# Optimization experiments

Hardware: AMD Instinct MI355X
Metric: run time of the kernel (lower is better)

Reference implementation:

```python
import jax, jax.numpy as jnp
import numpy as np

DELTA_V = 0.5
DELTA_D = 1.5
ALPHA = 1.0
BETA = 1.0
GAMMA = 0.001
K = 32          # max number of instance labels per image
EPS = 1e-12     # sqrt safety for masked/degenerate distances


def setup_inputs() -> dict:
    key = jax.random.key(0)
    k1, k2 = jax.random.split(key)
    B, F, H, W = 8, 32, 512, 512
    embeds = jax.random.normal(k1, (B, F, H, W), dtype=jnp.float32)
    labels = jax.random.randint(k2, (B, 1, H, W), 0, K, dtype=jnp.int32)
    return {"embeds": embeds, "labels": labels}


def _disc_loss(embeds, labels):
    B, F, H, W = embeds.shape
    N = H * W
    x = embeds.reshape(B, F, N)                     # [B,F,N]
    lab = labels.reshape(B, N)                      # [B,N]

    oh = jax.nn.one_hot(lab, K, dtype=x.dtype)      # [B,N,K]
    counts = oh.sum(axis=1)                         # [B,K] pixels per label
    present = counts > 0                            # [B,K]
    pres_f = present.astype(x.dtype)
    C = pres_f.sum(axis=-1)                         # [B] number of instances
    safe_counts = jnp.maximum(counts, 1.0)

    # per-label means (fused segment reduction as one GEMM)
    sums = jnp.einsum('bfn,bnk->bfk', x, oh)        # [B,F,K]
    mu = sums / safe_counts[:, None, :]             # [B,F,K]

    # --- variance (pull) term ---
    mu_pix = jnp.einsum('bfk,bnk->bfn', mu, oh)     # mean broadcast back to pixels
    d = jnp.sqrt(jnp.sum((mu_pix - x) ** 2, axis=1) + EPS)   # [B,N] ||mu_c - x||
    v = jnp.maximum(d - DELTA_V, 0.0) ** 2
    v_per = jnp.einsum('bn,bnk->bk', v, oh) / safe_counts    # per-label mean
    var_b = jnp.where(C > 0, (v_per * pres_f).sum(-1) / jnp.maximum(C, 1.0), 0.0)
    var_loss = var_b.sum()

    # --- distance (push) term: pairwise between cluster means ---
    diff = mu[:, :, :, None] - mu[:, :, None, :]    # [B,F,K,K]
    dist = jnp.sqrt(jnp.sum(diff ** 2, axis=1) + EPS)        # [B,K,K]
    pair = present[:, :, None] & present[:, None, :]
    upper = jnp.triu(jnp.ones((K, K), dtype=bool), k=1)      # ca < cb pairs
    pm = pair & upper[None]
    hinge = jnp.maximum(DELTA_D - dist, 0.0) ** 2
    dloss = jnp.where(pm, hinge, 0.0).sum(axis=(-1, -2))     # [B]
    denom = jnp.maximum(C * (C - 1.0), 1.0)
    dis_loss = jnp.where(C > 2, dloss / denom, 0.0).sum()

    # --- regularization term: sum of ||mu_c|| over present labels ---
    mu_norm = jnp.sqrt(jnp.sum(mu ** 2, axis=1) + EPS)       # [B,K]
    reg_b = jnp.where(C > 1, (mu_norm * pres_f).sum(-1), 0.0)
    reg_loss = reg_b.sum()

    return ALPHA * var_loss + BETA * dis_loss + GAMMA * reg_loss


def reference(embeds, labels):
    return _disc_loss(embeds, labels)
```

## Files before the change

### kernel.cpp

```cpp
#include <hip/hip_runtime.h>

#define KLAB 32
#define FDIM 32
#define NPIX (512 * 512)
#define BATCH 8
#define EPSF 1e-12f

typedef __attribute__((ext_vector_type(8))) short bf16x8;
typedef __attribute__((ext_vector_type(4))) short bf16x4;
typedef __attribute__((ext_vector_type(4))) float f32x4;

__device__ __forceinline__ short f2bf(float f) {
    unsigned u = __builtin_bit_cast(unsigned, f);
    unsigned r = (u + 0x7FFFu + ((u >> 16) & 1u)) >> 16;
    return (short)r;
}

__device__ __forceinline__ float bf2f(short s) {
    return __builtin_bit_cast(float, (unsigned)((unsigned short)s) << 16);
}

__global__ __launch_bounds__(256, 4) void k_msums(
    const float* __restrict__ x, const int* __restrict__ lab,
    float* __restrict__ g_sums, float* __restrict__ g_cnt,
    short* __restrict__ xbf)
{
    __shared__ __align__(16) short alds[2][32 * 256];
    __shared__ int lablds[2][256];

    const int tid = threadIdx.x;
    const int b = blockIdx.y;
    const int cx = blockIdx.x;
    const int w = tid >> 6, l = tid & 63;
    const int row = l & 15, grp = l >> 4;
    const size_t xb = (size_t)b * FDIM * NPIX;
    const size_t lb = (size_t)b * NPIX;
    const int bp0 = cx * 2048;

    const float* xw = x + xb + (size_t)(w * 8) * NPIX;
    short* xbw = xbf + xb + (size_t)(w * 8) * NPIX;

    f32x4 acc00{}, acc01{}, acc10{}, acc11{}, accC0{}, accC1{};
    bf16x8 ones;
#pragma unroll
    for (int j = 0; j < 8; ++j) ones[j] = (short)0x3F80;

    f32x4 sv[8];
    int slab;

    {
        const int sp = bp0;
#pragma unroll
        for (int r = 0; r < 8; ++r)
            sv[r] = *reinterpret_cast<const f32x4*>(xw + (size_t)r * NPIX + sp + l * 4);
        slab = lab[lb + sp + tid];
#pragma unroll
        for (int r = 0; r < 8; ++r) {
            bf16x4 c;
            c[0]=f2bf(sv[r].x); c[1]=f2bf(sv[r].y); c[2]=f2bf(sv[r].z); c[3]=f2bf(sv[r].w);
            *reinterpret_cast<bf16x4*>(xbw + (size_t)r * NPIX + sp + l * 4) = c;
            const int f = w * 8 + r;
            *reinterpret_cast<bf16x4*>((char*)&alds[0][0] + ((f * 512 + l * 8) ^ (r << 4))) = c;
        }
        lablds[0][tid] = slab;
    }
    __syncthreads();

#pragma unroll 1
    for (int t = 0; t < 8; ++t) {
        const int cb = t & 1, nb = cb ^ 1;

        if (t + 1 < 8) {
            const int sp = bp0 + (t + 1) * 256;
#pragma unroll
            for (int r = 0; r < 8; ++r)
                sv[r] = *reinterpret_cast<const f32x4*>(xw + (size_t)r * NPIX + sp + l * 4);
            slab = lab[lb + sp + tid];
        }

#pragma unroll
        for (int kq = 0; kq < 2; ++kq) {
            const int kk = 2 * w + kq;
            const int cbyte = (kk * 32 + grp * 8) * 2;
            const int swz = (row & 7) << 4;
            const bf16x8 a0 = *reinterpret_cast<const bf16x8*>(
                (char*)&alds[cb][0] + ((row * 512 + cbyte) ^ swz));
            const bf16x8 a1 = *reinterpret_cast<const bf16x8*>(
                (char*)&alds[cb][0] + (((row + 16) * 512 + cbyte) ^ swz));
            const int base = kk * 32 + grp * 8;
            const int4 la = *reinterpret_cast<const int4*>(&lablds[cb][base]);
            const int4 lc = *reinterpret_cast<const int4*>(&lablds[cb][base + 4]);
            bf16x8 b0, b1;
            const int lj[8] = {la.x, la.y, la.z, la.w, lc.x, lc.y, lc.z, lc.w};
#pragma unroll
            for (int j = 0; j < 8; ++j) {
                b0[j] = (lj[j] == row)      ? (short)0x3F80 : (short)0;
                b1[j] = (lj[j] == row + 16) ? (short)0x3F80 : (short)0;
            }
            acc00 = __builtin_amdgcn_mfma_f32_16x16x32_bf16(a0, b0, acc00, 0, 0, 0);
            acc10 = __builtin_amdgcn_mfma_f32_16x16x32_bf16(a1, b0, acc10, 0, 0, 0);
            acc01 = __builtin_amdgcn_mfma_f32_16x16x32_bf16(a0, b1, acc01, 0, 0, 0);
            acc11 = __builtin_amdgcn_mfma_f32_16x16x32_bf16(a1, b1, acc11, 0, 0, 0);
            accC0 = __builtin_amdgcn_mfma_f32_16x16x32_bf16(ones, b0, accC0, 0, 0, 0);
            accC1 = __builtin_amdgcn_mfma_f32_16x16x32_bf16(ones, b1, accC1, 0, 0, 0);
        }

        if (t + 1 < 8) {
            const int sp = bp0 + (t + 1) * 256;
#pragma unroll
            for (int r = 0; r < 8; ++r) {
                bf16x4 c;
                c[0]=f2bf(sv[r].x); c[1]=f2bf(sv[r].y); c[2]=f2bf(sv[r].z); c[3]=f2bf(sv[r].w);
                *reinterpret_cast<bf16x4*>(xbw + (size_t)r * NPIX + sp + l * 4) = c;
                const int f = w * 8 + r;
                *reinterpret_cast<bf16x4*>((char*)&alds[nb][0] + ((f * 512 + l * 8) ^ (r << 4))) = c;
            }
            lablds[nb][tid] = slab;
        }
        __syncthreads();
    }

    float* s_red = reinterpret_cast<float*>(&alds[0][0]);
#pragma unroll
    for (int i = 0; i < 4; ++i) {
        const int fr = grp * 4 + i;
        s_red[w * 1024 + (fr)      * KLAB + row]      = acc00[i];
        s_red[w * 1024 + (fr)      * KLAB + row + 16] = acc01[i];
        s_red[w * 1024 + (fr + 16) * KLAB + row]      = acc10[i];
        s_red[w * 1024 + (fr + 16) * KLAB + row + 16] = acc11[i];
    }
    __syncthreads();
    float* gs = g_sums + (size_t)b * FDIM * KLAB;
    for (int i = tid; i < FDIM * KLAB; i += 256)
        atomicAdd(&gs[i], s_red[i] + s_red[1024 + i] + s_red[2048 + i] + s_red[3072 + i]);
    if (l < 16) {
        atomicAdd(&g_cnt[b * KLAB + l],      accC0[0]);
        atomicAdd(&g_cnt[b * KLAB + l + 16], accC1[0]);
    }
}

__global__ __launch_bounds__(256) void k_var(
    const short* __restrict__ xbf, const int* __restrict__ lab,
    const float* __restrict__ g_sums, const float* __restrict__ g_cnt,
    float* __restrict__ g_vsum)
{
    __shared__ float mu_s[FDIM][KLAB];
    __shared__ float vloc[KLAB];
    const int tid = threadIdx.x;
    const int b = blockIdx.y;
    for (int i = tid; i < FDIM * KLAB; i += 256) {
        const int k = i & (KLAB - 1);
        (&mu_s[0][0])[i] = g_sums[(size_t)b * FDIM * KLAB + i] / fmaxf(g_cnt[b * KLAB + k], 1.f);
    }
    if (tid < KLAB) vloc[tid] = 0.f;
    __syncthreads();

    const int n0 = blockIdx.x * 1024 + tid * 4;
    const size_t lb = (size_t)b * NPIX;
    const int4 l4 = *reinterpret_cast<const int4*>(&lab[lb + n0]);
    const int k0 = l4.x & 31, k1 = l4.y & 31, k2 = l4.z & 31, k3 = l4.w & 31;
    const short* xp = xbf + (size_t)b * FDIM * NPIX + n0;

    bf16x4 sl[4];
#pragma unroll
    for (int f = 0; f < 4; ++f)
        sl[f] = *reinterpret_cast<const bf16x4*>(xp + (size_t)f * NPIX);

    float d0 = 0.f, d1 = 0.f, d2 = 0.f, d3 = 0.f;
#pragma unroll
    for (int f = 0; f < FDIM; ++f) {
        const bf16x4 cur = sl[f & 3];
        if (f + 4 < FDIM)
            sl[f & 3] = *reinterpret_cast<const bf16x4*>(xp + (size_t)(f + 4) * NPIX);
        const float* mf = &mu_s[f][0];
        float t;
        t = bf2f(cur[0]) - mf[k0]; d0 += t * t;
        t = bf2f(cur[1]) - mf[k1]; d1 += t * t;
        t = bf2f(cur[2]) - mf[k2]; d2 += t * t;
        t = bf2f(cur[3]) - mf[k3]; d3 += t * t;
    }
    float h;
    h = fmaxf(sqrtf(d0 + EPSF) - 0.5f, 0.f); atomicAdd(&vloc[k0], h * h);
    h = fmaxf(sqrtf(d1 + EPSF) - 0.5f, 0.f); atomicAdd(&vloc[k1], h * h);
    h = fmaxf(sqrtf(d2 + EPSF) - 0.5f, 0.f); atomicAdd(&vloc[k2], h * h);
    h = fmaxf(sqrtf(d3 + EPSF) - 0.5f, 0.f); atomicAdd(&vloc[k3], h * h);
    __syncthreads();
    if (tid < KLAB) atomicAdd(&g_vsum[b * KLAB + tid], vloc[tid]);
}

__global__ __launch_bounds__(256) void k_final(
    const float* __restrict__ g_sums, const float* __restrict__ g_cnt,
    const float* __restrict__ g_vsum, float* __restrict__ out)
{
    __shared__ float mu8[BATCH][FDIM][KLAB];
    __shared__ float cnt8[BATCH][KLAB];
    __shared__ float tot[BATCH];
    const int tid = threadIdx.x;
    const int l = tid & 63, w = tid >> 6;

    for (int i = tid; i < BATCH * FDIM * KLAB; i += 256) {
        const int bb = i >> 10, k = i & 31;
        (&mu8[0][0][0])[i] = g_sums[i] / fmaxf(g_cnt[bb * KLAB + k], 1.f);
    }
    (&cnt8[0][0])[tid] = g_cnt[tid];
    __syncthreads();

    for (int half = 0; half < 2; ++half) {
        const int bb = w + half * 4;
        float pres = 0.f, varp = 0.f, regp = 0.f, distp = 0.f;
        if (l < KLAB && cnt8[bb][l] > 0.f) {
            pres = 1.f;
            varp = g_vsum[bb * KLAB + l] / fmaxf(cnt8[bb][l], 1.f);
            float s = 0.f;
            for (int f = 0; f < FDIM; ++f) { float m = mu8[bb][f][l]; s += m * m; }
            regp = sqrtf(s + EPSF);
        }
        for (int p = l; p < KLAB * KLAB; p += 64) {
            const int i = p >> 5, j = p & 31;
            if (i < j && cnt8[bb][i] > 0.f && cnt8[bb][j] > 0.f) {
                float s = 0.f;
                for (int f = 0; f < FDIM; ++f) {
                    float d = mu8[bb][f][i] - mu8[bb][f][j]; s += d * d;
                }
                const float dist = sqrtf(s + EPSF);
                const float hg = fmaxf(1.5f - dist, 0.f);
                distp += hg * hg;
            }
        }
        for (int m = 32; m > 0; m >>= 1) {
            pres  += __shfl_xor(pres,  m, 64);
            varp  += __shfl_xor(varp,  m, 64);
            regp  += __shfl_xor(regp,  m, 64);
            distp += __shfl_xor(distp, m, 64);
        }
        if (l == 0) {
            const float C = pres;
            const float var_b = (C > 0.f) ? varp / fmaxf(C, 1.f) : 0.f;
            const float dis_b = (C > 2.f) ? distp / fmaxf(C * (C - 1.f), 1.f) : 0.f;
            const float reg_b = (C > 1.f) ? regp : 0.f;
            tot[bb] = var_b + dis_b + 0.001f * reg_b;
        }
    }
    __syncthreads();
    if (tid == 0) {
        float t = 0.f;
        for (int bb = 0; bb < BATCH; ++bb) t += tot[bb];
        out[0] = t;
    }
}

extern "C" void kernel_launch(void* const* d_in, const int* in_sizes, int n_in,
                              void* d_out, int out_size, void* d_ws, size_t ws_size,
                              hipStream_t stream) {
    const float* x = (const float*)d_in[0];
    const int* lab = (const int*)d_in[1];
    float* out = (float*)d_out;

    const size_t XBF_BYTES = (size_t)BATCH * FDIM * NPIX * 2;
    short* xbf    = (short*)d_ws;
    float* g_sums = (float*)((char*)d_ws + XBF_BYTES);
    float* g_cnt  = g_sums + (size_t)BATCH * FDIM * KLAB;
    float* g_vsum = g_cnt + (size_t)BATCH * KLAB;
    hipMemsetAsync(g_sums, 0, (size_t)(BATCH * FDIM * KLAB + 2 * BATCH * KLAB) * 4, stream);

    dim3 grid1(128, BATCH);
    k_msums<<<grid1, 256, 0, stream>>>(x, lab, g_sums, g_cnt, xbf);
    dim3 grid2(256, BATCH);
    k_var<<<grid2, 256, 0, stream>>>(xbf, lab, g_sums, g_cnt, g_vsum);
    k_final<<<1, 256, 0, stream>>>(g_sums, g_cnt, g_vsum, out);
}
```

Baseline: 148.7 us.

## Widen segment-sum blocks to 512 threads and defer bf16 global stores

The mean-sum kernel now uses 512-thread blocks that each cover 4096 pixels in 512-pixel tiles, with each wave loading 4 features over two 256-pixel halves, and the grid is halved accordingly. The bf16 copy of the input is now staged in registers and written to global memory at the start of the next iteration, so those stores can overlap with the loads and MFMA work. The final reduction sums eight wave partials before each atomic. This doubles LDS use per block and adds register pressure under the 512x4 launch bound, which may lower occupancy. The wave-to-row mapping in the MFMA stage is also reworked, along with the LDS swizzle.

```diff
diff --git a/kernel.cpp b/kernel.cpp
--- a/kernel.cpp
+++ b/kernel.cpp
@@ -20,13 +20,13 @@
     return __builtin_bit_cast(float, (unsigned)((unsigned short)s) << 16);
 }
 
-__global__ __launch_bounds__(256, 4) void k_msums(
+__global__ __launch_bounds__(512, 4) void k_msums(
     const float* __restrict__ x, const int* __restrict__ lab,
     float* __restrict__ g_sums, float* __restrict__ g_cnt,
     short* __restrict__ xbf)
 {
-    __shared__ __align__(16) short alds[2][32 * 256];
-    __shared__ int lablds[2][256];
+    __shared__ __align__(16) short alds[2][32 * 512];
+    __shared__ int lablds[2][512];
 
     const int tid = threadIdx.x;
     const int b = blockIdx.y;
@@ -35,10 +35,10 @@
     const int row = l & 15, grp = l >> 4;
     const size_t xb = (size_t)b * FDIM * NPIX;
     const size_t lb = (size_t)b * NPIX;
-    const int bp0 = cx * 2048;
-
-    const float* xw = x + xb + (size_t)(w * 8) * NPIX;
-    short* xbw = xbf + xb + (size_t)(w * 8) * NPIX;
+    const int bp0 = cx * 4096;
+
+    const float* xw = x + xb + (size_t)(w * 4) * NPIX;
+    short* xbw = xbf + xb + (size_t)(w * 4) * NPIX;
 
     f32x4 acc00{}, acc01{}, acc10{}, acc11{}, accC0{}, accC1{};
     bf16x8 ones;
@@ -46,22 +46,30 @@
     for (int j = 0; j < 8; ++j) ones[j] = (short)0x3F80;
 
     f32x4 sv[8];
+    bf16x4 st[8];
     int slab;
 
     {
         const int sp = bp0;
 #pragma unroll
-        for (int r = 0; r < 8; ++r)
-            sv[r] = *reinterpret_cast<const f32x4*>(xw + (size_t)r * NPIX + sp + l * 4);
+        for (int r = 0; r < 4; ++r)
+#pragma unroll
+            for (int j = 0; j < 2; ++j)
+                sv[r * 2 + j] = *reinterpret_cast<const f32x4*>(
+                    xw + (size_t)r * NPIX + sp + j * 256 + l * 4);
         slab = lab[lb + sp + tid];
 #pragma unroll
-        for (int r = 0; r < 8; ++r) {
-            bf16x4 c;
-            c[0]=f2bf(sv[r].x); c[1]=f2bf(sv[r].y); c[2]=f2bf(sv[r].z); c[3]=f2bf(sv[r].w);
-            *reinterpret_cast<bf16x4*>(xbw + (size_t)r * NPIX + sp + l * 4) = c;
-            const int f = w * 8 + r;
-            *reinterpret_cast<bf16x4*>((char*)&alds[0][0] + ((f * 512 + l * 8) ^ (r << 4))) = c;
-        }
+        for (int r = 0; r < 4; ++r)
+#pragma unroll
+            for (int j = 0; j < 2; ++j) {
+                const f32x4 v = sv[r * 2 + j];
+                bf16x4 c;
+                c[0]=f2bf(v.x); c[1]=f2bf(v.y); c[2]=f2bf(v.z); c[3]=f2bf(v.w);
+                st[r * 2 + j] = c;
+                const int f = w * 4 + r;
+                *reinterpret_cast<bf16x4*>((char*)&alds[0][0] +
+                    ((f * 1024 + j * 512 + l * 8) ^ ((f & 7) << 4))) = c;
+            }
         lablds[0][tid] = slab;
     }
     __syncthreads();
@@ -70,11 +78,24 @@
     for (int t = 0; t < 8; ++t) {
         const int cb = t & 1, nb = cb ^ 1;
 
+        {
+            const int sp = bp0 + t * 512;
+#pragma unroll
+            for (int r = 0; r < 4; ++r)
+#pragma unroll
+                for (int j = 0; j < 2; ++j)
+                    *reinterpret_cast<bf16x4*>(
+                        xbw + (size_t)r * NPIX + sp + j * 256 + l * 4) = st[r * 2 + j];
+        }
+
         if (t + 1 < 8) {
-            const int sp = bp0 + (t + 1) * 256;
-#pragma unroll
-            for (int r = 0; r < 8; ++r)
-                sv[r] = *reinterpret_cast<const f32x4*>(xw + (size_t)r * NPIX + sp + l * 4);
+            const int sp = bp0 + (t + 1) * 512;
+#pragma unroll
+            for (int r = 0; r < 4; ++r)
+#pragma unroll
+                for (int j = 0; j < 2; ++j)
+                    sv[r * 2 + j] = *reinterpret_cast<const f32x4*>(
+                        xw + (size_t)r * NPIX + sp + j * 256 + l * 4);
             slab = lab[lb + sp + tid];
         }
 
@@ -84,9 +105,9 @@
             const int cbyte = (kk * 32 + grp * 8) * 2;
             const int swz = (row & 7) << 4;
             const bf16x8 a0 = *reinterpret_cast<const bf16x8*>(
-                (char*)&alds[cb][0] + ((row * 512 + cbyte) ^ swz));
+                (char*)&alds[cb][0] + ((row * 1024 + cbyte) ^ swz));
             const bf16x8 a1 = *reinterpret_cast<const bf16x8*>(
-                (char*)&alds[cb][0] + (((row + 16) * 512 + cbyte) ^ swz));
+                (char*)&alds[cb][0] + (((row + 16) * 1024 + cbyte) ^ swz));
             const int base = kk * 32 + grp * 8;
             const int4 la = *reinterpret_cast<const int4*>(&lablds[cb][base]);
             const int4 lc = *reinterpret_cast<const int4*>(&lablds[cb][base + 4]);
@@ -106,15 +127,18 @@
         }
 
         if (t + 1 < 8) {
-            const int sp = bp0 + (t + 1) * 256;
-#pragma unroll
-            for (int r = 0; r < 8; ++r) {
-                bf16x4 c;
-                c[0]=f2bf(sv[r].x); c[1]=f2bf(sv[r].y); c[2]=f2bf(sv[r].z); c[3]=f2bf(sv[r].w);
-                *reinterpret_cast<bf16x4*>(xbw + (size_t)r * NPIX + sp + l * 4) = c;
-                const int f = w * 8 + r;
-                *reinterpret_cast<bf16x4*>((char*)&alds[nb][0] + ((f * 512 + l * 8) ^ (r << 4))) = c;
-            }
+#pragma unroll
+            for (int r = 0; r < 4; ++r)
+#pragma unroll
+                for (int j = 0; j < 2; ++j) {
+                    const f32x4 v = sv[r * 2 + j];
+                    bf16x4 c;
+                    c[0]=f2bf(v.x); c[1]=f2bf(v.y); c[2]=f2bf(v.z); c[3]=f2bf(v.w);
+                    st[r * 2 + j] = c;
+                    const int f = w * 4 + r;
+                    *reinterpret_cast<bf16x4*>((char*)&alds[nb][0] +
+                        ((f * 1024 + j * 512 + l * 8) ^ ((f & 7) << 4))) = c;
+                }
             lablds[nb][tid] = slab;
         }
         __syncthreads();
@@ -131,8 +155,12 @@
     }
     __syncthreads();
     float* gs = g_sums + (size_t)b * FDIM * KLAB;
-    for (int i = tid; i < FDIM * KLAB; i += 256)
-        atomicAdd(&gs[i], s_red[i] + s_red[1024 + i] + s_red[2048 + i] + s_red[3072 + i]);
+    for (int i = tid; i < FDIM * KLAB; i += 512) {
+        float s = 0.f;
+#pragma unroll
+        for (int ww = 0; ww < 8; ++ww) s += s_red[ww * 1024 + i];
+        atomicAdd(&gs[i], s);
+    }
     if (l < 16) {
         atomicAdd(&g_cnt[b * KLAB + l],      accC0[0]);
         atomicAdd(&g_cnt[b * KLAB + l + 16], accC1[0]);
@@ -263,8 +291,8 @@
     float* g_vsum = g_cnt + (size_t)BATCH * KLAB;
     hipMemsetAsync(g_sums, 0, (size_t)(BATCH * FDIM * KLAB + 2 * BATCH * KLAB) * 4, stream);
 
-    dim3 grid1(128, BATCH);
-    k_msums<<<grid1, 256, 0, stream>>>(x, lab, g_sums, g_cnt, xbf);
+    dim3 grid1(64, BATCH);
+    k_msums<<<grid1, 512, 0, stream>>>(x, lab, g_sums, g_cnt, xbf);
     dim3 grid2(256, BATCH);
     k_var<<<grid2, 256, 0, stream>>>(xbf, lab, g_sums, g_cnt, g_vsum);
     k_final<<<1, 256, 0, stream>>>(g_sums, g_cnt, g_vsum, out);
```

Measured after the change: 152.1 us. 2.3% more time.
